# Performance work log

Measured on AMD Instinct MI355X. Metric: run time of the kernel, lower is better.

Reference implementation:

```python
import jax, jax.numpy as jnp
import numpy as np

N_NODES = 100000
N_EDGES = 1600000
IN_FEATS = 64
OUT_FEATS = 64


def setup_inputs() -> dict:
    key = jax.random.key(0)
    k1, k2, k3, k4, k5 = jax.random.split(key, 5)
    h = jax.random.normal(k1, (N_NODES, IN_FEATS), dtype=jnp.float32)
    weight = jax.random.normal(k2, (IN_FEATS, OUT_FEATS), dtype=jnp.float32) * (1.0 / np.sqrt(OUT_FEATS))
    norm = jax.random.uniform(k3, (N_NODES, 1), dtype=jnp.float32)
    src = jax.random.randint(k4, (N_EDGES,), 0, N_NODES, dtype=jnp.int32)
    dst = jax.random.randint(k5, (N_EDGES,), 0, N_NODES, dtype=jnp.int32)
    return {"h": h, "weight": weight, "norm": norm, "src": src, "dst": dst}


def reference(h, weight, norm, src, dst):
    # GCN linear: [N, in] @ [in, out] -> [N, out]
    hw = jnp.matmul(h, weight)
    # pre-scale by source norm
    hn = hw * norm
    # gather messages at edge sources, scatter-sum into destinations
    msgs = hn[src]  # [E, out]
    agg = jax.ops.segment_sum(msgs, dst, num_segments=h.shape[0])
    # post-scale by destination norm
    return agg * norm
```

## Files before the change

### kernel.cpp

```cpp
#include <hip/hip_runtime.h>

#define N_NODES 100000
#define N_EDGES 1600000
#define F 64
#define NPB 128
#define NB ((N_NODES + NPB - 1) / NPB)
#define CAP 2432
#define BLK_E 8192
#define NSPLIT ((N_EDGES + BLK_E - 1) / BLK_E)
#define EPT (BLK_E / 512)
#define GEMM_ROWS 128
#define NGEMM ((N_NODES + GEMM_ROWS - 1) / GEMM_ROWS)

typedef unsigned short ushort_t;
typedef unsigned int uint_t;
using bf16x8 = __attribute__((ext_vector_type(8))) short;
using f32x4  = __attribute__((ext_vector_type(4))) float;

__device__ __forceinline__ ushort_t f2bf(float x) {
    uint_t u = __float_as_uint(x);
    u += 0x7FFFu + ((u >> 16) & 1u);
    return (ushort_t)(u >> 16);
}
__device__ __forceinline__ float bflo(uint_t v) {
    return __uint_as_float(v << 16);
}
__device__ __forceinline__ float bfhi(uint_t v) {
    return __uint_as_float(v & 0xFFFF0000u);
}

__device__ __forceinline__ int wave_iscan(int v) {
    const int lane = threadIdx.x & 63;
#pragma unroll
    for (int off = 1; off < 64; off <<= 1) {
        const int y = __shfl_up(v, off);
        if (lane >= off) v += y;
    }
    return v;
}
__device__ __forceinline__ int block_iscan(int v, int* wtot) {
    const int t = threadIdx.x;
    const int wv = t >> 6;
    const int ws = wave_iscan(v);
    if ((t & 63) == 63) wtot[wv] = ws;
    __syncthreads();
    int base = 0;
#pragma unroll
    for (int i = 0; i < 7; ++i)
        base += (i < wv) ? wtot[i] : 0;
    return base + ws;
}

__launch_bounds__(512)
__global__ void gemm_split_kernel(const float* __restrict__ h,
                                  const float* __restrict__ w,
                                  const float* __restrict__ norm,
                                  ushort_t* __restrict__ hn,
                                  const int* __restrict__ src,
                                  const int* __restrict__ dst,
                                  ushort_t* __restrict__ offtab,
                                  uint_t* __restrict__ seg) {
    __shared__ int hist[1024];
    __shared__ int base[NB + 2];
    __shared__ int wtot[8];
    const int t = threadIdx.x;

    if (blockIdx.x < NSPLIT) {
        const int e0 = blockIdx.x * BLK_E;
        const int n  = min(BLK_E, N_EDGES - e0);

        for (int i = t; i < 1024; i += 512) hist[i] = 0;
        __syncthreads();

        uint_t rec[EPT];
        short  bin[EPT];
        short  rnk[EPT];
#pragma unroll
        for (int j = 0; j < EPT; ++j) {
            const int idx = t + j * 512;
            if (idx < n) {
                const int d = dst[e0 + idx];
                const int s = src[e0 + idx];
                bin[j] = (short)(d >> 7);
                rec[j] = ((uint_t)s << 7) | (uint_t)(d & 127);
                rnk[j] = (short)atomicAdd(&hist[bin[j]], 1);
            } else {
                bin[j] = -1;
            }
        }
        __syncthreads();

        const int b0i = 2 * t;
        const int v0 = hist[b0i], v1 = hist[b0i + 1];
        const int ssum = v0 + v1;
        const int incl = block_iscan(ssum, wtot);
        int run = incl - ssum;
        ushort_t* offrow = offtab + (size_t)blockIdx.x * (NB + 1);
        const int vj[2] = {v0, v1};
#pragma unroll
        for (int j = 0; j < 2; ++j) {
            const int b = b0i + j;
            if (b < NB) {
                offrow[b] = (ushort_t)run;
                base[b] = run;
            } else if (b == NB) {
                offrow[NB] = (ushort_t)run;
            }
            run += vj[j];
        }
        __syncthreads();

        uint_t* myseg = seg + (size_t)blockIdx.x * BLK_E;
#pragma unroll
        for (int j = 0; j < EPT; ++j) {
            if (bin[j] >= 0)
                myseg[base[bin[j]] + rnk[j]] = rec[j];
        }
    } else {
        const int gb  = blockIdx.x - NSPLIT;
        const int wv  = t >> 6;
        const int l   = t & 63;
        const int lr  = l & 15;
        const int lk  = l >> 4;
        const int col = (wv & 3) * 16 + lr;
        const int r0  = gb * GEMM_ROWS + (wv >> 2) * 64;

        bf16x8 b0, b1;
#pragma unroll
        for (int j = 0; j < 8; ++j) {
            b0[j] = (short)f2bf(w[(lk * 8 + j) * F + col]);
            b1[j] = (short)f2bf(w[(32 + lk * 8 + j) * F + col]);
        }

        float4 hv[4][4];
#pragma unroll
        for (int tt = 0; tt < 4; ++tt) {
            const int r  = r0 + tt * 16 + lr;
            const int rl = min(r, N_NODES - 1);
            const float* hp = h + (size_t)rl * F + lk * 8;
            hv[tt][0] = *(const float4*)(hp);
            hv[tt][1] = *(const float4*)(hp + 4);
            hv[tt][2] = *(const float4*)(hp + 32);
            hv[tt][3] = *(const float4*)(hp + 36);
        }

        f32x4 accv[4];
#pragma unroll
        for (int tt = 0; tt < 4; ++tt) {
            bf16x8 a0, a1;
            a0[0] = (short)f2bf(hv[tt][0].x); a0[1] = (short)f2bf(hv[tt][0].y);
            a0[2] = (short)f2bf(hv[tt][0].z); a0[3] = (short)f2bf(hv[tt][0].w);
            a0[4] = (short)f2bf(hv[tt][1].x); a0[5] = (short)f2bf(hv[tt][1].y);
            a0[6] = (short)f2bf(hv[tt][1].z); a0[7] = (short)f2bf(hv[tt][1].w);
            a1[0] = (short)f2bf(hv[tt][2].x); a1[1] = (short)f2bf(hv[tt][2].y);
            a1[2] = (short)f2bf(hv[tt][2].z); a1[3] = (short)f2bf(hv[tt][2].w);
            a1[4] = (short)f2bf(hv[tt][3].x); a1[5] = (short)f2bf(hv[tt][3].y);
            a1[6] = (short)f2bf(hv[tt][3].z); a1[7] = (short)f2bf(hv[tt][3].w);

            f32x4 acc = {0.f, 0.f, 0.f, 0.f};
            acc = __builtin_amdgcn_mfma_f32_16x16x32_bf16(a0, b0, acc, 0, 0, 0);
            acc = __builtin_amdgcn_mfma_f32_16x16x32_bf16(a1, b1, acc, 0, 0, 0);
            accv[tt] = acc;
        }

#pragma unroll
        for (int tt = 0; tt < 4; ++tt) {
#pragma unroll
            for (int i2 = 0; i2 < 4; ++i2) {
                const int m = r0 + tt * 16 + lk * 4 + i2;
                if (m < N_NODES)
                    hn[(size_t)m * F + col] = f2bf(accv[tt][i2] * norm[m]);
            }
        }
    }
}

__launch_bounds__(512)
__global__ void gather_build_kernel(const ushort_t* __restrict__ offtab,
                                    const uint_t* __restrict__ seg,
                                    const ushort_t* __restrict__ hn,
                                    const float* __restrict__ norm,
                                    float* __restrict__ out) {
    __shared__ uint_t ebuf[CAP];
    __shared__ int    lsrc[CAP];
    __shared__ int    cnt[NPB];
    __shared__ int    beg[NPB];
    __shared__ int    cur[NPB];
    __shared__ int    sstart[NSPLIT];
    __shared__ int    sbase[NSPLIT];
    __shared__ int    slenA[NSPLIT];
    __shared__ int    wtot[8];
    __shared__ int    tot[1];

    const int b = blockIdx.x;
    const int t = threadIdx.x;

    int slen_v = 0, sstart_v = 0;
    if (t < NSPLIT) {
        const ushort_t* row = offtab + (size_t)t * (NB + 1);
        sstart_v = row[b];
        slen_v   = row[b + 1] - sstart_v;
        sstart[t] = sstart_v;
        slenA[t]  = slen_v;
    }
    if (t < NPB) cnt[t] = 0;

    const int incl = block_iscan(slen_v, wtot);
    if (t < NSPLIT) sbase[t] = incl - slen_v;
    if (t == 511) tot[0] = incl;
    __syncthreads();
    const int n = min(tot[0], CAP);

    const int grp    = t >> 4;
    const int lane16 = t & 15;
    for (int s = grp; s < NSPLIT; s += 32) {
        const int len  = slenA[s];
        const int base = sbase[s];
        const uint_t* sp = seg + (size_t)s * BLK_E + sstart[s];
        for (int j = lane16; j < len; j += 16) {
            const int o = base + j;
            if (o < CAP) {
                const uint_t v = sp[j];
                ebuf[o] = v;
                atomicAdd(&cnt[v & 127u], 1);
            }
        }
    }
    __syncthreads();

    const int cv = (t < NPB) ? cnt[t] : 0;
    const int incl2 = block_iscan(cv, wtot);
    if (t < NPB) {
        const int e = incl2 - cv;
        beg[t] = e;
        cur[t] = e;
    }
    __syncthreads();

    for (int i = t; i < n; i += 512) {
        const uint_t e = ebuf[i];
        const int p = atomicAdd(&cur[e & 127u], 1);
        lsrc[p] = (int)(e >> 7);
    }
    __syncthreads();

    const int wave = t >> 6;
    const int lane = t & 63;
    const int s = lane >> 4;
    const int c = lane & 15;

    for (int ld = wave; ld < NPB; ld += 8) {
        const int node = b * NPB + ld;
        if (node >= N_NODES) break;

        const int bg = beg[ld];
        const int en = bg + cnt[ld];

        float a0 = 0.f, a1 = 0.f, a2 = 0.f, a3 = 0.f;
        int i = bg;
        for (; i + 15 < en; i += 16) {
            const int sA = lsrc[i + s];
            const int sB = lsrc[i + 4 + s];
            const int sC = lsrc[i + 8 + s];
            const int sD = lsrc[i + 12 + s];
            const uint2 vA = *(const uint2*)(hn + (size_t)sA * F + 4 * c);
            const uint2 vB = *(const uint2*)(hn + (size_t)sB * F + 4 * c);
            const uint2 vC = *(const uint2*)(hn + (size_t)sC * F + 4 * c);
            const uint2 vD = *(const uint2*)(hn + (size_t)sD * F + 4 * c);
            a0 += bflo(vA.x) + bflo(vB.x) + bflo(vC.x) + bflo(vD.x);
            a1 += bfhi(vA.x) + bfhi(vB.x) + bfhi(vC.x) + bfhi(vD.x);
            a2 += bflo(vA.y) + bflo(vB.y) + bflo(vC.y) + bflo(vD.y);
            a3 += bfhi(vA.y) + bfhi(vB.y) + bfhi(vC.y) + bfhi(vD.y);
        }
        for (; i + 7 < en; i += 8) {
            const int sA = lsrc[i + s];
            const int sB = lsrc[i + 4 + s];
            const uint2 vA = *(const uint2*)(hn + (size_t)sA * F + 4 * c);
            const uint2 vB = *(const uint2*)(hn + (size_t)sB * F + 4 * c);
            a0 += bflo(vA.x) + bflo(vB.x);
            a1 += bfhi(vA.x) + bfhi(vB.x);
            a2 += bflo(vA.y) + bflo(vB.y);
            a3 += bfhi(vA.y) + bfhi(vB.y);
        }
        for (; i < en; i += 4) {
            const int e = i + s;
            if (e < en) {
                const int sv = lsrc[e];
                const uint2 v = *(const uint2*)(hn + (size_t)sv * F + 4 * c);
                a0 += bflo(v.x);
                a1 += bfhi(v.x);
                a2 += bflo(v.y);
                a3 += bfhi(v.y);
            }
        }

        a0 += __shfl_xor(a0, 16); a0 += __shfl_xor(a0, 32);
        a1 += __shfl_xor(a1, 16); a1 += __shfl_xor(a1, 32);
        a2 += __shfl_xor(a2, 16); a2 += __shfl_xor(a2, 32);
        a3 += __shfl_xor(a3, 16); a3 += __shfl_xor(a3, 32);

        if (s == 0) {
            const float nv = norm[node];
            float4 r;
            r.x = a0 * nv; r.y = a1 * nv; r.z = a2 * nv; r.w = a3 * nv;
            *(float4*)(out + (size_t)node * F + 4 * c) = r;
        }
    }
}

extern "C" void kernel_launch(void* const* d_in, const int* in_sizes, int n_in,
                              void* d_out, int out_size, void* d_ws, size_t ws_size,
                              hipStream_t stream) {
    const float* h    = (const float*)d_in[0];
    const float* w    = (const float*)d_in[1];
    const float* norm = (const float*)d_in[2];
    const int*   src  = (const int*)d_in[3];
    const int*   dst  = (const int*)d_in[4];
    float* out = (float*)d_out;

    char* ws = (char*)d_ws;
    ushort_t* hn     = (ushort_t*)ws;
    uint_t*   seg    = (uint_t*)(ws + 12800000);
    ushort_t* offtab = (ushort_t*)(ws + 12800000 + 6422528);

    gemm_split_kernel<<<NSPLIT + NGEMM, 512, 0, stream>>>(
        h, w, norm, hn, src, dst, offtab, seg);

    gather_build_kernel<<<NB, 512, 0, stream>>>(offtab, seg, hn, norm, out);
}
```

Baseline: 70.42 us.

## Aggregate int8-quantized features first, then apply GEMM per block after gather

Reorders the computation so raw features are scaled by source norm, quantized to int8 with a per-row scale, gathered and summed per destination, and only then multiplied by the weight with MFMA inside the gather kernel. This halves the bytes per gathered row relative to bf16 and removes the standalone GEMM pass. In exchange it adds per-row quantization error on the inputs and a bf16 round-trip of the aggregated values, which may affect accuracy tolerance. It also adds a 16 KB LDS tile per block, which may lower occupancy.

```diff
diff --git a/kernel.cpp b/kernel.cpp
--- a/kernel.cpp
+++ b/kernel.cpp
@@ -9,8 +9,7 @@
 #define BLK_E 8192
 #define NSPLIT ((N_EDGES + BLK_E - 1) / BLK_E)
 #define EPT (BLK_E / 512)
-#define GEMM_ROWS 128
-#define NGEMM ((N_NODES + GEMM_ROWS - 1) / GEMM_ROWS)
+#define NQ ((N_NODES + 63) / 64)
 
 typedef unsigned short ushort_t;
 typedef unsigned int uint_t;
@@ -22,11 +21,8 @@
     u += 0x7FFFu + ((u >> 16) & 1u);
     return (ushort_t)(u >> 16);
 }
-__device__ __forceinline__ float bflo(uint_t v) {
-    return __uint_as_float(v << 16);
-}
-__device__ __forceinline__ float bfhi(uint_t v) {
-    return __uint_as_float(v & 0xFFFF0000u);
+__device__ __forceinline__ float sx8(uint_t w, int b) {
+    return (float)((int)(w << (24 - 8 * b)) >> 24);
 }
 
 __device__ __forceinline__ int wave_iscan(int v) {
@@ -52,14 +48,14 @@
 }
 
 __launch_bounds__(512)
-__global__ void gemm_split_kernel(const float* __restrict__ h,
-                                  const float* __restrict__ w,
-                                  const float* __restrict__ norm,
-                                  ushort_t* __restrict__ hn,
-                                  const int* __restrict__ src,
-                                  const int* __restrict__ dst,
-                                  ushort_t* __restrict__ offtab,
-                                  uint_t* __restrict__ seg) {
+__global__ void quant_split_kernel(const float* __restrict__ h,
+                                   const float* __restrict__ norm,
+                                   signed char* __restrict__ gq,
+                                   float* __restrict__ gscale,
+                                   const int* __restrict__ src,
+                                   const int* __restrict__ dst,
+                                   ushort_t* __restrict__ offtab,
+                                   uint_t* __restrict__ seg) {
     __shared__ int hist[1024];
     __shared__ int base[NB + 2];
     __shared__ int wtot[8];
@@ -117,60 +113,32 @@
                 myseg[base[bin[j]] + rnk[j]] = rec[j];
         }
     } else {
-        const int gb  = blockIdx.x - NSPLIT;
-        const int wv  = t >> 6;
-        const int l   = t & 63;
-        const int lr  = l & 15;
-        const int lk  = l >> 4;
-        const int col = (wv & 3) * 16 + lr;
-        const int r0  = gb * GEMM_ROWS + (wv >> 2) * 64;
-
-        bf16x8 b0, b1;
-#pragma unroll
-        for (int j = 0; j < 8; ++j) {
-            b0[j] = (short)f2bf(w[(lk * 8 + j) * F + col]);
-            b1[j] = (short)f2bf(w[(32 + lk * 8 + j) * F + col]);
-        }
-
-        float4 hv[4][4];
-#pragma unroll
-        for (int tt = 0; tt < 4; ++tt) {
-            const int r  = r0 + tt * 16 + lr;
-            const int rl = min(r, N_NODES - 1);
-            const float* hp = h + (size_t)rl * F + lk * 8;
-            hv[tt][0] = *(const float4*)(hp);
-            hv[tt][1] = *(const float4*)(hp + 4);
-            hv[tt][2] = *(const float4*)(hp + 32);
-            hv[tt][3] = *(const float4*)(hp + 36);
-        }
-
-        f32x4 accv[4];
-#pragma unroll
-        for (int tt = 0; tt < 4; ++tt) {
-            bf16x8 a0, a1;
-            a0[0] = (short)f2bf(hv[tt][0].x); a0[1] = (short)f2bf(hv[tt][0].y);
-            a0[2] = (short)f2bf(hv[tt][0].z); a0[3] = (short)f2bf(hv[tt][0].w);
-            a0[4] = (short)f2bf(hv[tt][1].x); a0[5] = (short)f2bf(hv[tt][1].y);
-            a0[6] = (short)f2bf(hv[tt][1].z); a0[7] = (short)f2bf(hv[tt][1].w);
-            a1[0] = (short)f2bf(hv[tt][2].x); a1[1] = (short)f2bf(hv[tt][2].y);
-            a1[2] = (short)f2bf(hv[tt][2].z); a1[3] = (short)f2bf(hv[tt][2].w);
-            a1[4] = (short)f2bf(hv[tt][3].x); a1[5] = (short)f2bf(hv[tt][3].y);
-            a1[6] = (short)f2bf(hv[tt][3].z); a1[7] = (short)f2bf(hv[tt][3].w);
-
-            f32x4 acc = {0.f, 0.f, 0.f, 0.f};
-            acc = __builtin_amdgcn_mfma_f32_16x16x32_bf16(a0, b0, acc, 0, 0, 0);
-            acc = __builtin_amdgcn_mfma_f32_16x16x32_bf16(a1, b1, acc, 0, 0, 0);
-            accv[tt] = acc;
-        }
-
-#pragma unroll
-        for (int tt = 0; tt < 4; ++tt) {
-#pragma unroll
-            for (int i2 = 0; i2 < 4; ++i2) {
-                const int m = r0 + tt * 16 + lk * 4 + i2;
-                if (m < N_NODES)
-                    hn[(size_t)m * F + col] = f2bf(accv[tt][i2] * norm[m]);
-            }
+        const int qb  = blockIdx.x - NSPLIT;
+        const int row = qb * 64 + (t >> 3);
+        const int l8  = t & 7;
+        if (row < N_NODES) {
+            const float nv = norm[row];
+            const float4* hp = (const float4*)(h + (size_t)row * F + l8 * 8);
+            const float4 va = hp[0];
+            const float4 vb = hp[1];
+            float v[8] = {va.x * nv, va.y * nv, va.z * nv, va.w * nv,
+                          vb.x * nv, vb.y * nv, vb.z * nv, vb.w * nv};
+            float m = 0.f;
+#pragma unroll
+            for (int j = 0; j < 8; ++j) m = fmaxf(m, fabsf(v[j]));
+            m = fmaxf(m, __shfl_xor(m, 1));
+            m = fmaxf(m, __shfl_xor(m, 2));
+            m = fmaxf(m, __shfl_xor(m, 4));
+            const float inv = (m > 0.f) ? 127.f / m : 0.f;
+            uint_t lo = 0, hi = 0;
+#pragma unroll
+            for (int j = 0; j < 4; ++j) {
+                lo |= ((uint_t)(__float2int_rn(v[j] * inv) & 255)) << (8 * j);
+                hi |= ((uint_t)(__float2int_rn(v[4 + j] * inv) & 255)) << (8 * j);
+            }
+            uint2 pk; pk.x = lo; pk.y = hi;
+            *(uint2*)(gq + (size_t)row * F + l8 * 8) = pk;
+            if (l8 == 0) gscale[row] = (m > 0.f) ? m / 127.f : 0.f;
         }
     }
 }
@@ -178,19 +146,22 @@
 __launch_bounds__(512)
 __global__ void gather_build_kernel(const ushort_t* __restrict__ offtab,
                                     const uint_t* __restrict__ seg,
-                                    const ushort_t* __restrict__ hn,
+                                    const signed char* __restrict__ gq,
+                                    const float* __restrict__ gscale,
+                                    const float* __restrict__ w,
                                     const float* __restrict__ norm,
                                     float* __restrict__ out) {
-    __shared__ uint_t ebuf[CAP];
-    __shared__ int    lsrc[CAP];
-    __shared__ int    cnt[NPB];
-    __shared__ int    beg[NPB];
-    __shared__ int    cur[NPB];
-    __shared__ int    sstart[NSPLIT];
-    __shared__ int    sbase[NSPLIT];
-    __shared__ int    slenA[NSPLIT];
-    __shared__ int    wtot[8];
-    __shared__ int    tot[1];
+    __shared__ uint_t   ebuf[CAP];
+    __shared__ int      lsrc[CAP];
+    __shared__ int      cnt[NPB];
+    __shared__ int      beg[NPB];
+    __shared__ int      cur[NPB];
+    __shared__ int      sstart[NSPLIT];
+    __shared__ int      sbase[NSPLIT];
+    __shared__ int      slenA[NSPLIT];
+    __shared__ int      wtot[8];
+    __shared__ int      tot[1];
+    __shared__ ushort_t aggL[128 * 64];
 
     const int b = blockIdx.x;
     const int t = threadIdx.x;
@@ -215,10 +186,10 @@
     const int lane16 = t & 15;
     for (int s = grp; s < NSPLIT; s += 32) {
         const int len  = slenA[s];
-        const int base = sbase[s];
+        const int bas  = sbase[s];
         const uint_t* sp = seg + (size_t)s * BLK_E + sstart[s];
         for (int j = lane16; j < len; j += 16) {
-            const int o = base + j;
+            const int o = bas + j;
             if (o < CAP) {
                 const uint_t v = sp[j];
                 ebuf[o] = v;
@@ -246,8 +217,8 @@
 
     const int wave = t >> 6;
     const int lane = t & 63;
-    const int s = lane >> 4;
-    const int c = lane & 15;
+    const int s  = lane >> 3;
+    const int c8 = lane & 7;
 
     for (int ld = wave; ld < NPB; ld += 8) {
         const int node = b * NPB + ld;
@@ -257,53 +228,106 @@
         const int en = bg + cnt[ld];
 
         float a0 = 0.f, a1 = 0.f, a2 = 0.f, a3 = 0.f;
+        float a4 = 0.f, a5 = 0.f, a6 = 0.f, a7 = 0.f;
         int i = bg;
         for (; i + 15 < en; i += 16) {
             const int sA = lsrc[i + s];
-            const int sB = lsrc[i + 4 + s];
-            const int sC = lsrc[i + 8 + s];
-            const int sD = lsrc[i + 12 + s];
-            const uint2 vA = *(const uint2*)(hn + (size_t)sA * F + 4 * c);
-            const uint2 vB = *(const uint2*)(hn + (size_t)sB * F + 4 * c);
-            const uint2 vC = *(const uint2*)(hn + (size_t)sC * F + 4 * c);
-            const uint2 vD = *(const uint2*)(hn + (size_t)sD * F + 4 * c);
-            a0 += bflo(vA.x) + bflo(vB.x) + bflo(vC.x) + bflo(vD.x);
-            a1 += bfhi(vA.x) + bfhi(vB.x) + bfhi(vC.x) + bfhi(vD.x);
-            a2 += bflo(vA.y) + bflo(vB.y) + bflo(vC.y) + bflo(vD.y);
-            a3 += bfhi(vA.y) + bfhi(vB.y) + bfhi(vC.y) + bfhi(vD.y);
+            const int sB = lsrc[i + 8 + s];
+            const uint2 vA = *(const uint2*)(gq + (size_t)sA * F + c8 * 8);
+            const uint2 vB = *(const uint2*)(gq + (size_t)sB * F + c8 * 8);
+            const float cA = gscale[sA];
+            const float cB = gscale[sB];
+            a0 += cA * sx8(vA.x, 0) + cB * sx8(vB.x, 0);
+            a1 += cA * sx8(vA.x, 1) + cB * sx8(vB.x, 1);
+            a2 += cA * sx8(vA.x, 2) + cB * sx8(vB.x, 2);
+            a3 += cA * sx8(vA.x, 3) + cB * sx8(vB.x, 3);
+            a4 += cA * sx8(vA.y, 0) + cB * sx8(vB.y, 0);
+            a5 += cA * sx8(vA.y, 1) + cB * sx8(vB.y, 1);
+            a6 += cA * sx8(vA.y, 2) + cB * sx8(vB.y, 2);
+            a7 += cA * sx8(vA.y, 3) + cB * sx8(vB.y, 3);
         }
         for (; i + 7 < en; i += 8) {
             const int sA = lsrc[i + s];
-            const int sB = lsrc[i + 4 + s];
-            const uint2 vA = *(const uint2*)(hn + (size_t)sA * F + 4 * c);
-            const uint2 vB = *(const uint2*)(hn + (size_t)sB * F + 4 * c);
-            a0 += bflo(vA.x) + bflo(vB.x);
-            a1 += bfhi(vA.x) + bfhi(vB.x);
-            a2 += bflo(vA.y) + bflo(vB.y);
-            a3 += bfhi(vA.y) + bfhi(vB.y);
-        }
-        for (; i < en; i += 4) {
+            const uint2 vA = *(const uint2*)(gq + (size_t)sA * F + c8 * 8);
+            const float cA = gscale[sA];
+            a0 += cA * sx8(vA.x, 0);
+            a1 += cA * sx8(vA.x, 1);
+            a2 += cA * sx8(vA.x, 2);
+            a3 += cA * sx8(vA.x, 3);
+            a4 += cA * sx8(vA.y, 0);
+            a5 += cA * sx8(vA.y, 1);
+            a6 += cA * sx8(vA.y, 2);
+            a7 += cA * sx8(vA.y, 3);
+        }
+        if (i < en) {
             const int e = i + s;
             if (e < en) {
                 const int sv = lsrc[e];
-                const uint2 v = *(const uint2*)(hn + (size_t)sv * F + 4 * c);
-                a0 += bflo(v.x);
-                a1 += bfhi(v.x);
-                a2 += bflo(v.y);
-                a3 += bfhi(v.y);
-            }
-        }
-
-        a0 += __shfl_xor(a0, 16); a0 += __shfl_xor(a0, 32);
-        a1 += __shfl_xor(a1, 16); a1 += __shfl_xor(a1, 32);
-        a2 += __shfl_xor(a2, 16); a2 += __shfl_xor(a2, 32);
-        a3 += __shfl_xor(a3, 16); a3 += __shfl_xor(a3, 32);
+                const uint2 v = *(const uint2*)(gq + (size_t)sv * F + c8 * 8);
+                const float cc = gscale[sv];
+                a0 += cc * sx8(v.x, 0);
+                a1 += cc * sx8(v.x, 1);
+                a2 += cc * sx8(v.x, 2);
+                a3 += cc * sx8(v.x, 3);
+                a4 += cc * sx8(v.y, 0);
+                a5 += cc * sx8(v.y, 1);
+                a6 += cc * sx8(v.y, 2);
+                a7 += cc * sx8(v.y, 3);
+            }
+        }
+
+#pragma unroll
+        for (int off = 8; off < 64; off <<= 1) {
+            a0 += __shfl_xor(a0, off); a1 += __shfl_xor(a1, off);
+            a2 += __shfl_xor(a2, off); a3 += __shfl_xor(a3, off);
+            a4 += __shfl_xor(a4, off); a5 += __shfl_xor(a5, off);
+            a6 += __shfl_xor(a6, off); a7 += __shfl_xor(a7, off);
+        }
 
         if (s == 0) {
-            const float nv = norm[node];
-            float4 r;
-            r.x = a0 * nv; r.y = a1 * nv; r.z = a2 * nv; r.w = a3 * nv;
-            *(float4*)(out + (size_t)node * F + 4 * c) = r;
+            uint4 pk;
+            pk.x = (uint_t)f2bf(a0) | ((uint_t)f2bf(a1) << 16);
+            pk.y = (uint_t)f2bf(a2) | ((uint_t)f2bf(a3) << 16);
+            pk.z = (uint_t)f2bf(a4) | ((uint_t)f2bf(a5) << 16);
+            pk.w = (uint_t)f2bf(a6) | ((uint_t)f2bf(a7) << 16);
+            *(uint4*)(aggL + (size_t)ld * 64 + ((c8 ^ (ld & 7)) << 3)) = pk;
+        }
+    }
+    __syncthreads();
+
+    const int wv  = t >> 6;
+    const int l   = t & 63;
+    const int lr  = l & 15;
+    const int lk  = l >> 4;
+    const int col = (wv & 3) * 16 + lr;
+    const int mb  = (wv >> 2) * 64;
+
+    bf16x8 b0, b1;
+#pragma unroll
+    for (int j = 0; j < 8; ++j) {
+        b0[j] = (short)f2bf(w[(lk * 8 + j) * F + col]);
+        b1[j] = (short)f2bf(w[(32 + lk * 8 + j) * F + col]);
+    }
+
+    f32x4 accv[4];
+#pragma unroll
+    for (int tt = 0; tt < 4; ++tt) {
+        const int m = mb + tt * 16 + lr;
+        const bf16x8 fa0 = *(const bf16x8*)(aggL + (size_t)m * 64 + ((lk ^ (m & 7)) << 3));
+        const bf16x8 fa1 = *(const bf16x8*)(aggL + (size_t)m * 64 + (((lk + 4) ^ (m & 7)) << 3));
+        f32x4 acc = {0.f, 0.f, 0.f, 0.f};
+        acc = __builtin_amdgcn_mfma_f32_16x16x32_bf16(fa0, b0, acc, 0, 0, 0);
+        acc = __builtin_amdgcn_mfma_f32_16x16x32_bf16(fa1, b1, acc, 0, 0, 0);
+        accv[tt] = acc;
+    }
+
+#pragma unroll
+    for (int tt = 0; tt < 4; ++tt) {
+#pragma unroll
+        for (int i2 = 0; i2 < 4; ++i2) {
+            const int node = b * NPB + mb + tt * 16 + lk * 4 + i2;
+            if (node < N_NODES)
+                out[(size_t)node * F + col] = accv[tt][i2] * norm[node];
         }
     }
 }
@@ -319,12 +343,14 @@
     float* out = (float*)d_out;
 
     char* ws = (char*)d_ws;
-    ushort_t* hn     = (ushort_t*)ws;
-    uint_t*   seg    = (uint_t*)(ws + 12800000);
-    ushort_t* offtab = (ushort_t*)(ws + 12800000 + 6422528);
-
-    gemm_split_kernel<<<NSPLIT + NGEMM, 512, 0, stream>>>(
-        h, w, norm, hn, src, dst, offtab, seg);
-
-    gather_build_kernel<<<NB, 512, 0, stream>>>(offtab, seg, hn, norm, out);
-}
+    signed char* gq     = (signed char*)ws;
+    float*       gscale = (float*)(ws + 6400000);
+    uint_t*      seg    = (uint_t*)(ws + 6800128);
+    ushort_t*    offtab = (ushort_t*)(ws + 13222656);
+
+    quant_split_kernel<<<NSPLIT + NQ, 512, 0, stream>>>(
+        h, norm, gq, gscale, src, dst, offtab, seg);
+
+    gather_build_kernel<<<NB, 512, 0, stream>>>(
+        offtab, seg, gq, gscale, w, norm, out);
+}
```

Result: slower. 80.85 us (+14.8%).

## Use 1024-thread split/GEMM blocks and 16-byte gather loads with 8 lanes per row

Applied to the files above, without the earlier changes.

The first kernel moves to 1024-thread blocks, so each thread owns one histogram bin in the scan and the GEMM tile doubles to 256 rows. The gather stage now has each lane load 8 bf16 values (uint4) with 8 lanes covering a row, which halves the number of load instructions per edge and processes 8 edges per wave step instead of 4. The risks are higher register pressure and lower occupancy in the larger blocks, plus a wider shuffle reduction. The GEMM part, which is not shown, must correctly handle the new row mapping for 16 waves.

```diff
diff --git a/kernel.cpp b/kernel.cpp
--- a/kernel.cpp
+++ b/kernel.cpp
@@ -8,8 +8,8 @@
 #define CAP 2432
 #define BLK_E 8192
 #define NSPLIT ((N_EDGES + BLK_E - 1) / BLK_E)
-#define EPT (BLK_E / 512)
-#define GEMM_ROWS 128
+#define EPT (BLK_E / 1024)
+#define GEMM_ROWS 256
 #define NGEMM ((N_NODES + GEMM_ROWS - 1) / GEMM_ROWS)
 
 typedef unsigned short ushort_t;
@@ -38,6 +38,7 @@
     }
     return v;
 }
+template <int NW>
 __device__ __forceinline__ int block_iscan(int v, int* wtot) {
     const int t = threadIdx.x;
     const int wv = t >> 6;
@@ -46,12 +47,12 @@
     __syncthreads();
     int base = 0;
 #pragma unroll
-    for (int i = 0; i < 7; ++i)
+    for (int i = 0; i < NW - 1; ++i)
         base += (i < wv) ? wtot[i] : 0;
     return base + ws;
 }
 
-__launch_bounds__(512)
+__launch_bounds__(1024)
 __global__ void gemm_split_kernel(const float* __restrict__ h,
                                   const float* __restrict__ w,
                                   const float* __restrict__ norm,
@@ -61,15 +62,15 @@
                                   ushort_t* __restrict__ offtab,
                                   uint_t* __restrict__ seg) {
     __shared__ int hist[1024];
-    __shared__ int base[NB + 2];
-    __shared__ int wtot[8];
+    __shared__ int base[1024];
+    __shared__ int wtot[16];
     const int t = threadIdx.x;
 
     if (blockIdx.x < NSPLIT) {
         const int e0 = blockIdx.x * BLK_E;
         const int n  = min(BLK_E, N_EDGES - e0);
 
-        for (int i = t; i < 1024; i += 512) hist[i] = 0;
+        hist[t] = 0;
         __syncthreads();
 
         uint_t rec[EPT];
@@ -77,7 +78,7 @@
         short  rnk[EPT];
 #pragma unroll
         for (int j = 0; j < EPT; ++j) {
-            const int idx = t + j * 512;
+            const int idx = t + j * 1024;
             if (idx < n) {
                 const int d = dst[e0 + idx];
                 const int s = src[e0 + idx];
@@ -90,23 +91,15 @@
         }
         __syncthreads();
 
-        const int b0i = 2 * t;
-        const int v0 = hist[b0i], v1 = hist[b0i + 1];
-        const int ssum = v0 + v1;
-        const int incl = block_iscan(ssum, wtot);
-        int run = incl - ssum;
+        const int v = hist[t];
+        const int incl = block_iscan<16>(v, wtot);
+        const int run = incl - v;
         ushort_t* offrow = offtab + (size_t)blockIdx.x * (NB + 1);
-        const int vj[2] = {v0, v1};
-#pragma unroll
-        for (int j = 0; j < 2; ++j) {
-            const int b = b0i + j;
-            if (b < NB) {
-                offrow[b] = (ushort_t)run;
-                base[b] = run;
-            } else if (b == NB) {
-                offrow[NB] = (ushort_t)run;
-            }
-            run += vj[j];
+        if (t < NB) {
+            offrow[t] = (ushort_t)run;
+            base[t] = run;
+        } else if (t == NB) {
+            offrow[NB] = (ushort_t)run;
         }
         __syncthreads();
 
@@ -205,7 +198,7 @@
     }
     if (t < NPB) cnt[t] = 0;
 
-    const int incl = block_iscan(slen_v, wtot);
+    const int incl = block_iscan<8>(slen_v, wtot);
     if (t < NSPLIT) sbase[t] = incl - slen_v;
     if (t == 511) tot[0] = incl;
     __syncthreads();
@@ -215,10 +208,10 @@
     const int lane16 = t & 15;
     for (int s = grp; s < NSPLIT; s += 32) {
         const int len  = slenA[s];
-        const int base = sbase[s];
+        const int bas  = sbase[s];
         const uint_t* sp = seg + (size_t)s * BLK_E + sstart[s];
         for (int j = lane16; j < len; j += 16) {
-            const int o = base + j;
+            const int o = bas + j;
             if (o < CAP) {
                 const uint_t v = sp[j];
                 ebuf[o] = v;
@@ -229,7 +222,7 @@
     __syncthreads();
 
     const int cv = (t < NPB) ? cnt[t] : 0;
-    const int incl2 = block_iscan(cv, wtot);
+    const int incl2 = block_iscan<8>(cv, wtot);
     if (t < NPB) {
         const int e = incl2 - cv;
         beg[t] = e;
@@ -246,8 +239,8 @@
 
     const int wave = t >> 6;
     const int lane = t & 63;
-    const int s = lane >> 4;
-    const int c = lane & 15;
+    const int s  = lane >> 3;
+    const int c8 = lane & 7;
 
     for (int ld = wave; ld < NPB; ld += 8) {
         const int node = b * NPB + ld;
@@ -257,53 +250,66 @@
         const int en = bg + cnt[ld];
 
         float a0 = 0.f, a1 = 0.f, a2 = 0.f, a3 = 0.f;
+        float a4 = 0.f, a5 = 0.f, a6 = 0.f, a7 = 0.f;
         int i = bg;
         for (; i + 15 < en; i += 16) {
             const int sA = lsrc[i + s];
-            const int sB = lsrc[i + 4 + s];
-            const int sC = lsrc[i + 8 + s];
-            const int sD = lsrc[i + 12 + s];
-            const uint2 vA = *(const uint2*)(hn + (size_t)sA * F + 4 * c);
-            const uint2 vB = *(const uint2*)(hn + (size_t)sB * F + 4 * c);
-            const uint2 vC = *(const uint2*)(hn + (size_t)sC * F + 4 * c);
-            const uint2 vD = *(const uint2*)(hn + (size_t)sD * F + 4 * c);
-            a0 += bflo(vA.x) + bflo(vB.x) + bflo(vC.x) + bflo(vD.x);
-            a1 += bfhi(vA.x) + bfhi(vB.x) + bfhi(vC.x) + bfhi(vD.x);
-            a2 += bflo(vA.y) + bflo(vB.y) + bflo(vC.y) + bflo(vD.y);
-            a3 += bfhi(vA.y) + bfhi(vB.y) + bfhi(vC.y) + bfhi(vD.y);
-        }
-        for (; i + 7 < en; i += 8) {
-            const int sA = lsrc[i + s];
-            const int sB = lsrc[i + 4 + s];
-            const uint2 vA = *(const uint2*)(hn + (size_t)sA * F + 4 * c);
-            const uint2 vB = *(const uint2*)(hn + (size_t)sB * F + 4 * c);
+            const int sB = lsrc[i + 8 + s];
+            const uint4 vA = *(const uint4*)(hn + (size_t)sA * F + c8 * 8);
+            const uint4 vB = *(const uint4*)(hn + (size_t)sB * F + c8 * 8);
             a0 += bflo(vA.x) + bflo(vB.x);
             a1 += bfhi(vA.x) + bfhi(vB.x);
             a2 += bflo(vA.y) + bflo(vB.y);
             a3 += bfhi(vA.y) + bfhi(vB.y);
-        }
-        for (; i < en; i += 4) {
+            a4 += bflo(vA.z) + bflo(vB.z);
+            a5 += bfhi(vA.z) + bfhi(vB.z);
+            a6 += bflo(vA.w) + bflo(vB.w);
+            a7 += bfhi(vA.w) + bfhi(vB.w);
+        }
+        for (; i + 7 < en; i += 8) {
+            const int sA = lsrc[i + s];
+            const uint4 vA = *(const uint4*)(hn + (size_t)sA * F + c8 * 8);
+            a0 += bflo(vA.x);
+            a1 += bfhi(vA.x);
+            a2 += bflo(vA.y);
+            a3 += bfhi(vA.y);
+            a4 += bflo(vA.z);
+            a5 += bfhi(vA.z);
+            a6 += bflo(vA.w);
+            a7 += bfhi(vA.w);
+        }
+        if (i < en) {
             const int e = i + s;
             if (e < en) {
                 const int sv = lsrc[e];
-                const uint2 v = *(const uint2*)(hn + (size_t)sv * F + 4 * c);
+                const uint4 v = *(const uint4*)(hn + (size_t)sv * F + c8 * 8);
                 a0 += bflo(v.x);
                 a1 += bfhi(v.x);
                 a2 += bflo(v.y);
                 a3 += bfhi(v.y);
+                a4 += bflo(v.z);
+                a5 += bfhi(v.z);
+                a6 += bflo(v.w);
+                a7 += bfhi(v.w);
             }
         }
 
-        a0 += __shfl_xor(a0, 16); a0 += __shfl_xor(a0, 32);
-        a1 += __shfl_xor(a1, 16); a1 += __shfl_xor(a1, 32);
-        a2 += __shfl_xor(a2, 16); a2 += __shfl_xor(a2, 32);
-        a3 += __shfl_xor(a3, 16); a3 += __shfl_xor(a3, 32);
+#pragma unroll
+        for (int off = 8; off < 64; off <<= 1) {
+            a0 += __shfl_xor(a0, off); a1 += __shfl_xor(a1, off);
+            a2 += __shfl_xor(a2, off); a3 += __shfl_xor(a3, off);
+            a4 += __shfl_xor(a4, off); a5 += __shfl_xor(a5, off);
+            a6 += __shfl_xor(a6, off); a7 += __shfl_xor(a7, off);
+        }
 
         if (s == 0) {
             const float nv = norm[node];
-            float4 r;
-            r.x = a0 * nv; r.y = a1 * nv; r.z = a2 * nv; r.w = a3 * nv;
-            *(float4*)(out + (size_t)node * F + 4 * c) = r;
+            float4 r0v, r1v;
+            r0v.x = a0 * nv; r0v.y = a1 * nv; r0v.z = a2 * nv; r0v.w = a3 * nv;
+            r1v.x = a4 * nv; r1v.y = a5 * nv; r1v.z = a6 * nv; r1v.w = a7 * nv;
+            float* op = out + (size_t)node * F + c8 * 8;
+            *(float4*)(op)     = r0v;
+            *(float4*)(op + 4) = r1v;
         }
     }
 }
@@ -323,7 +329,7 @@
     uint_t*   seg    = (uint_t*)(ws + 12800000);
     ushort_t* offtab = (ushort_t*)(ws + 12800000 + 6422528);
 
-    gemm_split_kernel<<<NSPLIT + NGEMM, 512, 0, stream>>>(
+    gemm_split_kernel<<<NSPLIT + NGEMM, 1024, 0, stream>>>(
         h, w, norm, hn, src, dst, offtab, seg);
 
     gather_build_kernel<<<NB, 512, 0, stream>>>(offtab, seg, hn, norm, out);
```

Measured after the change: 86.32 us. +22.6%, slower.
